# Optimization experiments

Hardware: AMD Instinct MI355X
Metric: run time of the kernel (lower is better)

The kernel has to match this reference:

```python
import jax, jax.numpy as jnp
import numpy as np

CAPACITY_FACTOR = 1.25


def setup_inputs() -> dict:
    key = jax.random.key(0)
    k1, k2, k3, k4, k5, k6 = jax.random.split(key, 6)
    N, d, E, h = 8192, 1024, 8, 2816
    x = jax.random.normal(k1, (N, d), dtype=jnp.float32)
    topK_indices = jax.random.randint(k2, (N,), 0, E, dtype=jnp.int64)
    topK_scores = jax.random.uniform(k3, (N,), dtype=jnp.float32)
    Wg = jax.random.normal(k4, (E, d, h), dtype=jnp.float32) * 0.02
    Wu = jax.random.normal(k5, (E, d, h), dtype=jnp.float32) * 0.02
    Wd = jax.random.normal(k6, (E, h, d), dtype=jnp.float32) * 0.02
    return {"x": x, "topK_indices": topK_indices, "topK_scores": topK_scores,
            "Wg": Wg, "Wu": Wu, "Wd": Wd}


def reference(x, topK_indices, topK_scores, Wg, Wu, Wd):
    # x: [N, d] tokens; topK_indices: [N] top-1 expert ids; per-expert SwiGLU FFN.
    N, d = x.shape
    E = Wg.shape[0]
    capacity = int(CAPACITY_FACTOR * N / E)  # = 1280

    idx = topK_indices.astype(jnp.int32)
    onehot = jax.nn.one_hot(idx, E, dtype=jnp.int32)            # [N, E]
    # position of each token within its expert's queue (first-come-first-served)
    pos = jnp.sum((jnp.cumsum(onehot, axis=0) - 1) * onehot, axis=1)  # [N]
    kept = pos < capacity                                        # dropped tokens pass through

    # flat dispatch slot: expert*capacity + pos for kept tokens, overflow bucket otherwise
    slots = jnp.where(kept, idx * capacity + pos, E * capacity)  # [N]
    buf = jnp.zeros((E * capacity + 1, d), dtype=x.dtype).at[slots].set(x)
    xe = buf[: E * capacity].reshape(E, capacity, d)             # [E, C, d]

    # per-expert SwiGLU FFN (grouped GEMMs)
    hgate = jnp.einsum('ecd,edh->ech', xe, Wg)
    hup = jnp.einsum('ecd,edh->ech', xe, Wu)
    hact = jax.nn.silu(hgate) * hup
    out = jnp.einsum('ech,ehd->ecd', hact, Wd).reshape(E * capacity, d)
    out = jnp.concatenate([out, jnp.zeros((1, d), out.dtype)], axis=0)

    y_tok = out[slots]                                           # gather back per token
    # multiply_gate_scores=True: scale expert output by routing score; dropped -> identity
    y = jnp.where(kept[:, None], y_tok * topK_scores[:, None], x)
    return y
```

## Files before the change

kernel.cpp:

```cpp
#include <hip/hip_runtime.h>
#include <cstdint>
#include <cstddef>

#define N_TOK 8192
#define DIM   1024
#define NEXP  8
#define HID   2816
#define CAP   1280

typedef __bf16 bf16x8 __attribute__((ext_vector_type(8)));
typedef float  floatx4 __attribute__((ext_vector_type(4)));
typedef unsigned short u16x8 __attribute__((ext_vector_type(8)));

__device__ __forceinline__ unsigned short f2bf(float f) {
  return __builtin_bit_cast(unsigned short, (__bf16)f);
}

__device__ __forceinline__ void async16(void* lds, const void* g) {
  __builtin_amdgcn_global_load_lds(
      (const __attribute__((address_space(1))) void*)g,
      (__attribute__((address_space(3))) void*)lds, 16, 0, 0);
}

__device__ __forceinline__ void fence_barrier() {
  asm volatile("" ::: "memory");
  __builtin_amdgcn_s_barrier();
  asm volatile("" ::: "memory");
}

__device__ __forceinline__ floatx4 mfma16(bf16x8 a, bf16x8 b, floatx4 c) {
  return __builtin_amdgcn_mfma_f32_16x16x32_bf16(a, b, c, 0, 0, 0);
}

__global__ void route_kernel(const int* __restrict__ idx, int idx_stride,
                             int* __restrict__ slot,
                             int* __restrict__ slot_token,
                             int* __restrict__ counts) {
  __shared__ int hist[256][NEXP];
  const int t = threadIdx.x;
  int loc[NEXP];
#pragma unroll
  for (int e = 0; e < NEXP; e++) loc[e] = 0;
  const int base = t * 32;
  for (int i = 0; i < 32; i++) {
    int e = idx[(base + i) * idx_stride];
    loc[e]++;
  }
#pragma unroll
  for (int e = 0; e < NEXP; e++) hist[t][e] = loc[e];
  __syncthreads();
  if (t < NEXP) {
    int run = 0;
    for (int i = 0; i < 256; i++) { int v = hist[i][t]; hist[i][t] = run; run += v; }
    counts[t] = run < CAP ? run : CAP;
  }
  __syncthreads();
  int b2[NEXP];
#pragma unroll
  for (int e = 0; e < NEXP; e++) b2[e] = hist[t][e];
  for (int i = 0; i < 32; i++) {
    const int n = base + i;
    const int e = idx[n * idx_stride];
    const int p = b2[e]++;
    if (p < CAP) {
      const int s = e * CAP + p;
      slot[n] = s;
      slot_token[s] = n;
    } else {
      slot[n] = -1;
    }
  }
}

__global__ void dispatch_kernel(const float* __restrict__ x,
                                const int* __restrict__ slot,
                                unsigned short* __restrict__ xe,
                                float* __restrict__ y) {
  const int n = blockIdx.x;
  const int t = threadIdx.x;
  const int s = slot[n];
  const float4 v = ((const float4*)(x + (size_t)n * DIM))[t];
  if (s >= 0) {
    ushort4 b;
    b.x = f2bf(v.x); b.y = f2bf(v.y); b.z = f2bf(v.z); b.w = f2bf(v.w);
    ((ushort4*)(xe + (size_t)s * DIM))[t] = b;
  } else {
    ((float4*)(y + (size_t)n * DIM))[t] = v;
  }
}

__global__ __launch_bounds__(256)
void transpose_cvt(const float* __restrict__ in,
                   unsigned short* __restrict__ out,
                   const int R, const int C) {
  __shared__ float tile[64][65];
  const int e = blockIdx.z;
  const float* ib = in + (size_t)e * R * C;
  unsigned short* ob = out + (size_t)e * R * C;
  const int t = threadIdx.x;
  const int c0 = blockIdx.x * 64, r0 = blockIdx.y * 64;
  const int lr = t >> 4;
  const int lc = (t & 15) * 4;
#pragma unroll
  for (int i = 0; i < 4; i++) {
    const float4 v = *(const float4*)(ib + (size_t)(r0 + lr + i * 16) * C + c0 + lc);
    tile[lr + i * 16][lc + 0] = v.x;
    tile[lr + i * 16][lc + 1] = v.y;
    tile[lr + i * 16][lc + 2] = v.z;
    tile[lr + i * 16][lc + 3] = v.w;
  }
  __syncthreads();
  const int oc = t >> 2;
  const int sub = t & 3;
#pragma unroll
  for (int half = 0; half < 2; half++) {
    const int rch = sub + half * 4;
    u16x8 o;
#pragma unroll
    for (int j = 0; j < 8; j++) o[j] = f2bf(tile[rch * 8 + j][oc]);
    *(u16x8*)(ob + (size_t)(c0 + oc) * R + r0 + rch * 8) = o;
  }
}

__global__ __launch_bounds__(512, 2)
void gateup_gemm2(const unsigned short* __restrict__ A,
                  const unsigned short* __restrict__ Bg,
                  const unsigned short* __restrict__ Bu,
                  const int* __restrict__ counts,
                  unsigned short* __restrict__ hact) {
  extern __shared__ __align__(16) char smem[];
  const int bid = blockIdx.x;
  const int xcd = bid & 7;
  const int slotb = bid >> 3;
  const int m = slotb % 5;
  const int cgl = slotb / 5;
  const int cg = xcd + 8 * cgl;
  const int n = cg % 22;
  const int e = cg / 22;

  const int cnt = counts[e];
  const int m0 = m * 256;
  if (m0 >= cnt) return;
  const int n0 = n * 128;

  const int t = threadIdx.x;
  const int lane = t & 63;
  const int w = t >> 6;
  const int wr = w >> 2;
  const int wc = w & 3;
  const int li = lane & 15;
  const int q = lane >> 4;

  const int sr8 = t >> 3;
  const int cLog = (t & 7) ^ (sr8 & 7);
  const unsigned short* aB  = A  + ((size_t)e * CAP + m0 + sr8) * DIM + cLog * 8;
  const unsigned short* bgB = Bg + ((size_t)e * HID + n0 + sr8) * DIM + cLog * 8;
  const unsigned short* buB = Bu + ((size_t)e * HID + n0 + sr8) * DIM + cLog * 8;

  auto stageU = [&](int bb, int uoff, const unsigned short* s0, const unsigned short* s1) {
    async16(smem + bb * 65536 + uoff + t * 16, s0);
    async16(smem + bb * 65536 + uoff + 8192 + t * 16, s1);
  };

  const int rowA = (wr * 64 + li) * 128;
  const int rowB = (wc * 32 + li) * 128;
  const int c0 = (q ^ (li & 7)) * 16;

  floatx4 accg[8][2] = {};
  floatx4 accu[8][2] = {};

  constexpr int NT = DIM / 64;

  stageU(0, 0,     aB,                     aB + (size_t)64 * DIM);
  stageU(0, 32768, bgB,                    bgB + (size_t)64 * DIM);
  stageU(0, 49152, buB,                    buB + (size_t)64 * DIM);
  stageU(0, 16384, aB + (size_t)128 * DIM, aB + (size_t)192 * DIM);
  stageU(1, 0,     aB + 64,                aB + (size_t)64 * DIM + 64);
  asm volatile("s_waitcnt vmcnt(4)" ::: "memory");
  fence_barrier();

#pragma unroll 2
  for (int T = 0; T < NT; T++) {
    const int b = T & 1;
    const int bn = b ^ 1;
    char* sb = smem + b * 65536;
    bf16x8 bgf[2][2], buf2[2][2];
    {
      bf16x8 af[4][2];
#pragma unroll
      for (int mi = 0; mi < 4; mi++) {
        af[mi][0] = *(const bf16x8*)(sb + rowA + mi * 2048 + c0);
        af[mi][1] = *(const bf16x8*)(sb + rowA + mi * 2048 + (c0 ^ 64));
      }
#pragma unroll
      for (int ni = 0; ni < 2; ni++) {
        bgf[ni][0]  = *(const bf16x8*)(sb + 32768 + rowB + ni * 2048 + c0);
        bgf[ni][1]  = *(const bf16x8*)(sb + 32768 + rowB + ni * 2048 + (c0 ^ 64));
        buf2[ni][0] = *(const bf16x8*)(sb + 49152 + rowB + ni * 2048 + c0);
        buf2[ni][1] = *(const bf16x8*)(sb + 49152 + rowB + ni * 2048 + (c0 ^ 64));
      }
      if (T + 1 < NT) {
        stageU(bn, 32768, bgB + (T + 1) * 64, bgB + (size_t)64 * DIM + (T + 1) * 64);
        stageU(bn, 49152, buB + (T + 1) * 64, buB + (size_t)64 * DIM + (T + 1) * 64);
      }
      asm volatile("" ::: "memory");
      __builtin_amdgcn_s_barrier();
      asm volatile("s_waitcnt lgkmcnt(0)" ::: "memory");
      __builtin_amdgcn_sched_barrier(0);
      __builtin_amdgcn_s_setprio(1);
#pragma unroll
      for (int mi = 0; mi < 4; mi++)
#pragma unroll
        for (int ni = 0; ni < 2; ni++) {
          accg[mi][ni] = mfma16(af[mi][0], bgf[ni][0], accg[mi][ni]);
          accg[mi][ni] = mfma16(af[mi][1], bgf[ni][1], accg[mi][ni]);
          accu[mi][ni] = mfma16(af[mi][0], buf2[ni][0], accu[mi][ni]);
          accu[mi][ni] = mfma16(af[mi][1], buf2[ni][1], accu[mi][ni]);
        }
      __builtin_amdgcn_s_setprio(0);
      if (T + 1 < NT) asm volatile("s_waitcnt vmcnt(6)" ::: "memory");
      else            asm volatile("s_waitcnt vmcnt(0)" ::: "memory");
      fence_barrier();
    }
    {
      bf16x8 af[4][2];
#pragma unroll
      for (int mi = 0; mi < 4; mi++) {
        af[mi][0] = *(const bf16x8*)(sb + 16384 + rowA + mi * 2048 + c0);
        af[mi][1] = *(const bf16x8*)(sb + 16384 + rowA + mi * 2048 + (c0 ^ 64));
      }
      if (T + 1 < NT)
        stageU(bn, 16384, aB + (size_t)128 * DIM + (T + 1) * 64,
                          aB + (size_t)192 * DIM + (T + 1) * 64);
      if (T + 2 < NT)
        stageU(b, 0, aB + (T + 2) * 64, aB + (size_t)64 * DIM + (T + 2) * 64);
      asm volatile("" ::: "memory");
      __builtin_amdgcn_s_barrier();
      asm volatile("s_waitcnt lgkmcnt(0)" ::: "memory");
      __builtin_amdgcn_sched_barrier(0);
      __builtin_amdgcn_s_setprio(1);
#pragma unroll
      for (int mi = 0; mi < 4; mi++)
#pragma unroll
        for (int ni = 0; ni < 2; ni++) {
          accg[4 + mi][ni] = mfma16(af[mi][0], bgf[ni][0], accg[4 + mi][ni]);
          accg[4 + mi][ni] = mfma16(af[mi][1], bgf[ni][1], accg[4 + mi][ni]);
          accu[4 + mi][ni] = mfma16(af[mi][0], buf2[ni][0], accu[4 + mi][ni]);
          accu[4 + mi][ni] = mfma16(af[mi][1], buf2[ni][1], accu[4 + mi][ni]);
        }
      __builtin_amdgcn_s_setprio(0);
      if (T + 2 < NT)      asm volatile("s_waitcnt vmcnt(4)" ::: "memory");
      else if (T + 1 < NT) asm volatile("s_waitcnt vmcnt(2)" ::: "memory");
      fence_barrier();
    }
  }

  unsigned short* ob = hact + (size_t)e * CAP * HID;
#pragma unroll
  for (int mh = 0; mh < 2; mh++)
#pragma unroll
    for (int mi = 0; mi < 4; mi++)
#pragma unroll
      for (int r = 0; r < 4; r++) {
        const int row = m0 + mh * 128 + wr * 64 + mi * 16 + q * 4 + r;
        const size_t rb = (size_t)row * HID;
#pragma unroll
        for (int ni = 0; ni < 2; ni++) {
          const int col = n0 + wc * 32 + ni * 16 + li;
          const float g = accg[mh * 4 + mi][ni][r];
          const float u = accu[mh * 4 + mi][ni][r];
          ob[rb + col] = f2bf(g / (1.0f + __expf(-g)) * u);
        }
      }
}

__global__ __launch_bounds__(256, 2)
void down_gemm2(const unsigned short* __restrict__ A,
                const unsigned short* __restrict__ Bt,
                const int* __restrict__ counts,
                const int* __restrict__ slot_token,
                const float* __restrict__ scores,
                float* __restrict__ y) {
  extern __shared__ __align__(16) char smem[];
  const int bid = blockIdx.x;
  const int xcd = bid & 7;
  const int slotb = bid >> 3;
  const int m = slotb % 10;
  const int cgl = slotb / 10;
  const int cg = xcd + 8 * cgl;
  const int n = cg % 8;
  const int e = cg / 8;

  const int cnt = counts[e];
  const int m0 = m * 128;
  if (m0 >= cnt) return;
  const int n0 = n * 128;

  const int t = threadIdx.x;
  const int lane = t & 63;
  const int w = t >> 6;
  const int wr = w >> 1;
  const int wc = w & 1;
  const int li = lane & 15;
  const int q = lane >> 4;

  const int sr8 = t >> 3;
  const int cLog = (t & 7) ^ (sr8 & 7);
  const unsigned short* aB = A  + ((size_t)e * CAP + m0 + sr8) * HID + cLog * 8;
  const unsigned short* bB = Bt + ((size_t)e * DIM + n0 + sr8) * HID + cLog * 8;

  auto stageA = [&](int bb, int koff) {
#pragma unroll
    for (int j = 0; j < 4; j++)
      async16(smem + bb * 32768 + j * 4096 + t * 16, aB + (size_t)j * 32 * HID + koff);
  };
  auto stageB = [&](int bb, int koff) {
#pragma unroll
    for (int j = 0; j < 4; j++)
      async16(smem + bb * 32768 + 16384 + j * 4096 + t * 16, bB + (size_t)j * 32 * HID + koff);
  };

  const int rowA = (wr * 64 + li) * 128;
  const int rowB = (wc * 64 + li) * 128;
  const int c0 = (q ^ (li & 7)) * 16;

  floatx4 acc[4][4] = {};

  constexpr int NT = HID / 64;

  stageA(0, 0);
  stageB(0, 0);
  stageA(1, 64);
  asm volatile("s_waitcnt vmcnt(4)" ::: "memory");
  fence_barrier();

#pragma unroll 2
  for (int T = 0; T < NT; T++) {
    const int b = T & 1;
    const int bn = b ^ 1;
    char* sb = smem + b * 32768;
    bf16x8 af[4][2], bfr[4][2];
#pragma unroll
    for (int mi = 0; mi < 4; mi++) {
      af[mi][0] = *(const bf16x8*)(sb + rowA + mi * 2048 + c0);
      af[mi][1] = *(const bf16x8*)(sb + rowA + mi * 2048 + (c0 ^ 64));
    }
#pragma unroll
    for (int ni = 0; ni < 4; ni++) {
      bfr[ni][0] = *(const bf16x8*)(sb + 16384 + rowB + ni * 2048 + c0);
      bfr[ni][1] = *(const bf16x8*)(sb + 16384 + rowB + ni * 2048 + (c0 ^ 64));
    }
    if (T + 1 < NT) stageB(bn, (T + 1) * 64);
    asm volatile("" ::: "memory");
    __builtin_amdgcn_s_barrier();
    asm volatile("s_waitcnt lgkmcnt(0)" ::: "memory");
    __builtin_amdgcn_sched_barrier(0);
    __builtin_amdgcn_s_setprio(1);
#pragma unroll
    for (int mi = 0; mi < 4; mi++)
#pragma unroll
      for (int ni = 0; ni < 4; ni++) {
        acc[mi][ni] = mfma16(af[mi][0], bfr[ni][0], acc[mi][ni]);
        acc[mi][ni] = mfma16(af[mi][1], bfr[ni][1], acc[mi][ni]);
      }
    __builtin_amdgcn_s_setprio(0);
    if (T + 2 < NT) stageA(b, (T + 2) * 64);
    if (T + 2 < NT)      asm volatile("s_waitcnt vmcnt(4)" ::: "memory");
    else if (T + 1 < NT) asm volatile("s_waitcnt vmcnt(0)" ::: "memory");
    fence_barrier();
  }

#pragma unroll
  for (int mi = 0; mi < 4; mi++)
#pragma unroll
    for (int r = 0; r < 4; r++) {
      const int row = m0 + wr * 64 + mi * 16 + q * 4 + r;
      if (row < cnt) {
        const int tok = slot_token[e * CAP + row];
        const float s = scores[tok];
        float* yr = y + (size_t)tok * DIM;
#pragma unroll
        for (int ni = 0; ni < 4; ni++) {
          const int col = n0 + wc * 64 + ni * 16 + li;
          yr[col] = acc[mi][ni][r] * s;
        }
      }
    }
}

extern "C" void kernel_launch(void* const* d_in, const int* in_sizes, int n_in,
                              void* d_out, int out_size, void* d_ws, size_t ws_size,
                              hipStream_t stream) {
  const float* x      = (const float*)d_in[0];
  const int*   idx    = (const int*)d_in[1];
  const float* scores = (const float*)d_in[2];
  const float* Wg     = (const float*)d_in[3];
  const float* Wu     = (const float*)d_in[4];
  const float* Wd     = (const float*)d_in[5];
  float* y = (float*)d_out;

  const int idx_stride = (in_sizes[1] == 2 * N_TOK) ? 2 : 1;

  char* ws = (char*)d_ws;
  size_t off = 0;
  auto alloc = [&](size_t b) -> char* {
    char* p = ws + off;
    off += (b + 255) & ~(size_t)255;
    return p;
  };
  int* counts            = (int*)alloc(NEXP * 4);
  int* slot              = (int*)alloc((size_t)N_TOK * 4);
  int* slot_token        = (int*)alloc((size_t)NEXP * CAP * 4);
  unsigned short* xe     = (unsigned short*)alloc((size_t)NEXP * CAP * DIM * 2);
  unsigned short* hact   = (unsigned short*)alloc((size_t)NEXP * CAP * HID * 2);
  unsigned short* wg_t   = (unsigned short*)alloc((size_t)NEXP * DIM * HID * 2);
  unsigned short* wu_t   = (unsigned short*)alloc((size_t)NEXP * DIM * HID * 2);
  unsigned short* wd_t   = (unsigned short*)alloc((size_t)NEXP * DIM * HID * 2);
  (void)ws_size; (void)n_in; (void)out_size;

  static bool s_attr_done = false;
  if (!s_attr_done) {
    hipFuncSetAttribute((const void*)gateup_gemm2,
                        hipFuncAttributeMaxDynamicSharedMemorySize, 131072);
    hipFuncSetAttribute((const void*)down_gemm2,
                        hipFuncAttributeMaxDynamicSharedMemorySize, 65536);
    s_attr_done = true;
  }

  route_kernel<<<1, 256, 0, stream>>>(idx, idx_stride, slot, slot_token, counts);
  dispatch_kernel<<<N_TOK, 256, 0, stream>>>(x, slot, xe, y);

  transpose_cvt<<<dim3(HID / 64, DIM / 64, NEXP), 256, 0, stream>>>(Wg, wg_t, DIM, HID);
  transpose_cvt<<<dim3(HID / 64, DIM / 64, NEXP), 256, 0, stream>>>(Wu, wu_t, DIM, HID);
  transpose_cvt<<<dim3(DIM / 64, HID / 64, NEXP), 256, 0, stream>>>(Wd, wd_t, HID, DIM);

  gateup_gemm2<<<8 * 22 * 5, 512, 131072, stream>>>(xe, wg_t, wu_t, counts, hact);
  down_gemm2<<<8 * 8 * 10, 256, 65536, stream>>>(hact, wd_t, counts, slot_token, scores, y);
}
```

Measured before the change: 549.0 us.

## Stage GEMM B tiles through registers and parallelize routing prefix scan

Both GEMM kernels now load the weight (B) tiles into registers two iterations ahead and write them to LDS themselves, instead of using direct global-to-LDS async loads. Only the A tiles keep the async path, and the vmcnt waits and barriers are retuned to match. The routing kernel replaces its serial 256-step per-expert prefix loop with a parallel Hillis-Steele scan across threads, and avoids dynamic register indexing. The intent is to cut the serial routing latency and hide weight-load latency better, at the cost of more VGPR pressure and extra LDS write instructions in the main loop.

```diff
diff --git a/kernel.cpp b/kernel.cpp
--- a/kernel.cpp
+++ b/kernel.cpp
@@ -43,25 +43,43 @@
   for (int e = 0; e < NEXP; e++) loc[e] = 0;
   const int base = t * 32;
   for (int i = 0; i < 32; i++) {
-    int e = idx[(base + i) * idx_stride];
-    loc[e]++;
-  }
-#pragma unroll
-  for (int e = 0; e < NEXP; e++) hist[t][e] = loc[e];
+    const int e = idx[(base + i) * idx_stride];
+#pragma unroll
+    for (int k = 0; k < NEXP; k++) loc[k] += (e == k) ? 1 : 0;
+  }
+  int v[NEXP];
+#pragma unroll
+  for (int e = 0; e < NEXP; e++) { v[e] = loc[e]; hist[t][e] = loc[e]; }
   __syncthreads();
+  for (int d = 1; d < 256; d <<= 1) {
+    int nb[NEXP];
+    const bool has = (t >= d);
+    if (has) {
+#pragma unroll
+      for (int e = 0; e < NEXP; e++) nb[e] = hist[t - d][e];
+    }
+    __syncthreads();
+    if (has) {
+#pragma unroll
+      for (int e = 0; e < NEXP; e++) { v[e] += nb[e]; hist[t][e] = v[e]; }
+    }
+    __syncthreads();
+  }
   if (t < NEXP) {
-    int run = 0;
-    for (int i = 0; i < 256; i++) { int v = hist[i][t]; hist[i][t] = run; run += v; }
-    counts[t] = run < CAP ? run : CAP;
-  }
-  __syncthreads();
+    const int tot = hist[255][t];
+    counts[t] = tot < CAP ? tot : CAP;
+  }
   int b2[NEXP];
 #pragma unroll
-  for (int e = 0; e < NEXP; e++) b2[e] = hist[t][e];
+  for (int e = 0; e < NEXP; e++) b2[e] = v[e] - loc[e];
   for (int i = 0; i < 32; i++) {
     const int n = base + i;
     const int e = idx[n * idx_stride];
-    const int p = b2[e]++;
+    int p = 0;
+#pragma unroll
+    for (int k = 0; k < NEXP; k++) {
+      if (e == k) { p = b2[k]; b2[k] = p + 1; }
+    }
     if (p < CAP) {
       const int s = e * CAP + p;
       slot[n] = s;
@@ -123,7 +141,7 @@
 }
 
 __global__ __launch_bounds__(512, 2)
-void gateup_gemm2(const unsigned short* __restrict__ A,
+void gateup_gemm3(const unsigned short* __restrict__ A,
                   const unsigned short* __restrict__ Bg,
                   const unsigned short* __restrict__ Bu,
                   const int* __restrict__ counts,
@@ -171,17 +189,32 @@
 
   constexpr int NT = DIM / 64;
 
-  stageU(0, 0,     aB,                     aB + (size_t)64 * DIM);
-  stageU(0, 32768, bgB,                    bgB + (size_t)64 * DIM);
-  stageU(0, 49152, buB,                    buB + (size_t)64 * DIM);
-  stageU(0, 16384, aB + (size_t)128 * DIM, aB + (size_t)192 * DIM);
-  stageU(1, 0,     aB + 64,                aB + (size_t)64 * DIM + 64);
-  asm volatile("s_waitcnt vmcnt(4)" ::: "memory");
-  fence_barrier();
-
-#pragma unroll 2
-  for (int T = 0; T < NT; T++) {
-    const int b = T & 1;
+  uint4 rg0[4], rg1[4];
+
+  {
+    rg0[0] = *(const uint4*)(bgB);
+    rg0[1] = *(const uint4*)(bgB + (size_t)64 * DIM);
+    rg0[2] = *(const uint4*)(buB);
+    rg0[3] = *(const uint4*)(buB + (size_t)64 * DIM);
+    rg1[0] = *(const uint4*)(bgB + 64);
+    rg1[1] = *(const uint4*)(bgB + (size_t)64 * DIM + 64);
+    rg1[2] = *(const uint4*)(buB + 64);
+    rg1[3] = *(const uint4*)(buB + (size_t)64 * DIM + 64);
+    __builtin_amdgcn_sched_barrier(0);
+    stageU(0, 0,     aB,                     aB + (size_t)64 * DIM);
+    stageU(0, 16384, aB + (size_t)128 * DIM, aB + (size_t)192 * DIM);
+    stageU(1, 0,     aB + 64,                aB + (size_t)64 * DIM + 64);
+    asm volatile("s_waitcnt vmcnt(10)" ::: "memory");
+    *(uint4*)(smem + 32768 + t * 16)        = rg0[0];
+    *(uint4*)(smem + 32768 + 8192 + t * 16) = rg0[1];
+    *(uint4*)(smem + 49152 + t * 16)        = rg0[2];
+    *(uint4*)(smem + 49152 + 8192 + t * 16) = rg0[3];
+    asm volatile("s_waitcnt vmcnt(4)" ::: "memory");
+    asm volatile("s_waitcnt lgkmcnt(0)" ::: "memory");
+    fence_barrier();
+  }
+
+  auto body = [&](int T, int b, uint4 (&rgOld)[4], uint4 (&rgNew)[4]) {
     const int bn = b ^ 1;
     char* sb = smem + b * 65536;
     bf16x8 bgf[2][2], buf2[2][2];
@@ -199,12 +232,14 @@
         buf2[ni][0] = *(const bf16x8*)(sb + 49152 + rowB + ni * 2048 + c0);
         buf2[ni][1] = *(const bf16x8*)(sb + 49152 + rowB + ni * 2048 + (c0 ^ 64));
       }
-      if (T + 1 < NT) {
-        stageU(bn, 32768, bgB + (T + 1) * 64, bgB + (size_t)64 * DIM + (T + 1) * 64);
-        stageU(bn, 49152, buB + (T + 1) * 64, buB + (size_t)64 * DIM + (T + 1) * 64);
-      }
-      asm volatile("" ::: "memory");
-      __builtin_amdgcn_s_barrier();
+      if (T + 2 < NT) {
+        rgNew[0] = *(const uint4*)(bgB + (T + 2) * 64);
+        rgNew[1] = *(const uint4*)(bgB + (size_t)64 * DIM + (T + 2) * 64);
+        rgNew[2] = *(const uint4*)(buB + (T + 2) * 64);
+        rgNew[3] = *(const uint4*)(buB + (size_t)64 * DIM + (T + 2) * 64);
+      }
+      __builtin_amdgcn_sched_barrier(0);
+      fence_barrier();
       asm volatile("s_waitcnt lgkmcnt(0)" ::: "memory");
       __builtin_amdgcn_sched_barrier(0);
       __builtin_amdgcn_s_setprio(1);
@@ -218,8 +253,9 @@
           accu[mi][ni] = mfma16(af[mi][1], buf2[ni][1], accu[mi][ni]);
         }
       __builtin_amdgcn_s_setprio(0);
-      if (T + 1 < NT) asm volatile("s_waitcnt vmcnt(6)" ::: "memory");
-      else            asm volatile("s_waitcnt vmcnt(0)" ::: "memory");
+      if (T + 2 < NT)      asm volatile("s_waitcnt vmcnt(6)" ::: "memory");
+      else if (T + 1 < NT) asm volatile("s_waitcnt vmcnt(2)" ::: "memory");
+      else                 asm volatile("s_waitcnt vmcnt(0)" ::: "memory");
       fence_barrier();
     }
     {
@@ -228,14 +264,21 @@
       for (int mi = 0; mi < 4; mi++) {
         af[mi][0] = *(const bf16x8*)(sb + 16384 + rowA + mi * 2048 + c0);
         af[mi][1] = *(const bf16x8*)(sb + 16384 + rowA + mi * 2048 + (c0 ^ 64));
+      }
+      if (T + 1 < NT) {
+        char* db = smem + bn * 65536;
+        *(uint4*)(db + 32768 + t * 16)        = rgOld[0];
+        *(uint4*)(db + 32768 + 8192 + t * 16) = rgOld[1];
+        *(uint4*)(db + 49152 + t * 16)        = rgOld[2];
+        *(uint4*)(db + 49152 + 8192 + t * 16) = rgOld[3];
       }
       if (T + 1 < NT)
         stageU(bn, 16384, aB + (size_t)128 * DIM + (T + 1) * 64,
                           aB + (size_t)192 * DIM + (T + 1) * 64);
       if (T + 2 < NT)
         stageU(b, 0, aB + (T + 2) * 64, aB + (size_t)64 * DIM + (T + 2) * 64);
-      asm volatile("" ::: "memory");
-      __builtin_amdgcn_s_barrier();
+      __builtin_amdgcn_sched_barrier(0);
+      fence_barrier();
       asm volatile("s_waitcnt lgkmcnt(0)" ::: "memory");
       __builtin_amdgcn_sched_barrier(0);
       __builtin_amdgcn_s_setprio(1);
@@ -249,10 +292,15 @@
           accu[4 + mi][ni] = mfma16(af[mi][1], buf2[ni][1], accu[4 + mi][ni]);
         }
       __builtin_amdgcn_s_setprio(0);
-      if (T + 2 < NT)      asm volatile("s_waitcnt vmcnt(4)" ::: "memory");
+      if (T + 2 < NT)      asm volatile("s_waitcnt vmcnt(8)" ::: "memory");
       else if (T + 1 < NT) asm volatile("s_waitcnt vmcnt(2)" ::: "memory");
       fence_barrier();
     }
+  };
+
+  for (int T = 0; T < NT; T += 2) {
+    body(T,     0, rg1, rg0);
+    body(T + 1, 1, rg0, rg1);
   }
 
   unsigned short* ob = hact + (size_t)e * CAP * HID;
@@ -275,7 +323,7 @@
 }
 
 __global__ __launch_bounds__(256, 2)
-void down_gemm2(const unsigned short* __restrict__ A,
+void down_gemm3(const unsigned short* __restrict__ A,
                 const unsigned short* __restrict__ Bt,
                 const int* __restrict__ counts,
                 const int* __restrict__ slot_token,
@@ -314,11 +362,6 @@
     for (int j = 0; j < 4; j++)
       async16(smem + bb * 32768 + j * 4096 + t * 16, aB + (size_t)j * 32 * HID + koff);
   };
-  auto stageB = [&](int bb, int koff) {
-#pragma unroll
-    for (int j = 0; j < 4; j++)
-      async16(smem + bb * 32768 + 16384 + j * 4096 + t * 16, bB + (size_t)j * 32 * HID + koff);
-  };
 
   const int rowA = (wr * 64 + li) * 128;
   const int rowB = (wc * 64 + li) * 128;
@@ -328,15 +371,28 @@
 
   constexpr int NT = HID / 64;
 
-  stageA(0, 0);
-  stageB(0, 0);
-  stageA(1, 64);
-  asm volatile("s_waitcnt vmcnt(4)" ::: "memory");
-  fence_barrier();
-
-#pragma unroll 2
-  for (int T = 0; T < NT; T++) {
-    const int b = T & 1;
+  uint4 rg0[4], rg1[4];
+
+  {
+#pragma unroll
+    for (int j = 0; j < 4; j++)
+      rg0[j] = *(const uint4*)(bB + (size_t)j * 32 * HID);
+#pragma unroll
+    for (int j = 0; j < 4; j++)
+      rg1[j] = *(const uint4*)(bB + (size_t)j * 32 * HID + 64);
+    __builtin_amdgcn_sched_barrier(0);
+    stageA(0, 0);
+    stageA(1, 64);
+    asm volatile("s_waitcnt vmcnt(12)" ::: "memory");
+#pragma unroll
+    for (int j = 0; j < 4; j++)
+      *(uint4*)(smem + 16384 + j * 4096 + t * 16) = rg0[j];
+    asm volatile("s_waitcnt vmcnt(4)" ::: "memory");
+    asm volatile("s_waitcnt lgkmcnt(0)" ::: "memory");
+    fence_barrier();
+  }
+
+  auto body = [&](int T, int b, uint4 (&rgOld)[4], uint4 (&rgNew)[4]) {
     const int bn = b ^ 1;
     char* sb = smem + b * 32768;
     bf16x8 af[4][2], bfr[4][2];
@@ -350,9 +406,19 @@
       bfr[ni][0] = *(const bf16x8*)(sb + 16384 + rowB + ni * 2048 + c0);
       bfr[ni][1] = *(const bf16x8*)(sb + 16384 + rowB + ni * 2048 + (c0 ^ 64));
     }
-    if (T + 1 < NT) stageB(bn, (T + 1) * 64);
-    asm volatile("" ::: "memory");
-    __builtin_amdgcn_s_barrier();
+    if (T + 2 < NT) {
+#pragma unroll
+      for (int j = 0; j < 4; j++)
+        rgNew[j] = *(const uint4*)(bB + (size_t)j * 32 * HID + (T + 2) * 64);
+    }
+    if (T + 1 < NT) {
+      char* db = smem + bn * 32768;
+#pragma unroll
+      for (int j = 0; j < 4; j++)
+        *(uint4*)(db + 16384 + j * 4096 + t * 16) = rgOld[j];
+    }
+    __builtin_amdgcn_sched_barrier(0);
+    fence_barrier();
     asm volatile("s_waitcnt lgkmcnt(0)" ::: "memory");
     __builtin_amdgcn_sched_barrier(0);
     __builtin_amdgcn_s_setprio(1);
@@ -365,9 +431,14 @@
       }
     __builtin_amdgcn_s_setprio(0);
     if (T + 2 < NT) stageA(b, (T + 2) * 64);
-    if (T + 2 < NT)      asm volatile("s_waitcnt vmcnt(4)" ::: "memory");
+    if (T + 2 < NT)      asm volatile("s_waitcnt vmcnt(8)" ::: "memory");
     else if (T + 1 < NT) asm volatile("s_waitcnt vmcnt(0)" ::: "memory");
     fence_barrier();
+  };
+
+  for (int T = 0; T < NT; T += 2) {
+    body(T,     0, rg1, rg0);
+    body(T + 1, 1, rg0, rg1);
   }
 
 #pragma unroll
@@ -420,9 +491,9 @@
 
   static bool s_attr_done = false;
   if (!s_attr_done) {
-    hipFuncSetAttribute((const void*)gateup_gemm2,
+    hipFuncSetAttribute((const void*)gateup_gemm3,
                         hipFuncAttributeMaxDynamicSharedMemorySize, 131072);
-    hipFuncSetAttribute((const void*)down_gemm2,
+    hipFuncSetAttribute((const void*)down_gemm3,
                         hipFuncAttributeMaxDynamicSharedMemorySize, 65536);
     s_attr_done = true;
   }
@@ -434,6 +505,6 @@
   transpose_cvt<<<dim3(HID / 64, DIM / 64, NEXP), 256, 0, stream>>>(Wu, wu_t, DIM, HID);
   transpose_cvt<<<dim3(DIM / 64, HID / 64, NEXP), 256, 0, stream>>>(Wd, wd_t, HID, DIM);
 
-  gateup_gemm2<<<8 * 22 * 5, 512, 131072, stream>>>(xe, wg_t, wu_t, counts, hact);
-  down_gemm2<<<8 * 8 * 10, 256, 65536, stream>>>(hact, wd_t, counts, slot_token, scores, y);
-}
+  gateup_gemm3<<<8 * 22 * 5, 512, 131072, stream>>>(xe, wg_t, wu_t, counts, hact);
+  down_gemm3<<<8 * 8 * 10, 256, 65536, stream>>>(hact, wd_t, counts, slot_token, scores, y);
+}
```

After: 925.8 us. 1.69x slower.
